# Performance work log

Measured on AMD Instinct MI355X. Metric: run time of the kernel, lower is better.

Reference implementation:

```python
import jax, jax.numpy as jnp
import numpy as np

B, S, HID, NH, DH = 2, 1024, 4096, 32, 128
ACT_BITS, W_BITS = 8, 4
NEG_INF = float(np.finfo(np.float32).min)


def _qdq(x, bits):
    """Symmetric fake-quant over the last axis (per-token / per-out-channel), with STE."""
    qmax = 2.0 ** (bits - 1) - 1
    s = jnp.maximum(jnp.max(jnp.abs(x), axis=-1, keepdims=True) / qmax, 1e-8)
    q = jnp.clip(jnp.round(x / s), -qmax - 1, qmax) * s
    return x + jax.lax.stop_gradient(q - x)


def _rope_tables(seq_len, dim):
    inv_freq = 1.0 / (10000.0 ** (np.arange(0, dim, 2, dtype=np.float32) / dim))
    t = np.arange(seq_len, dtype=np.float32)
    freqs = np.outer(t, inv_freq)              # [S, DH/2]
    emb = np.concatenate([freqs, freqs], -1)   # [S, DH]
    return jnp.asarray(np.cos(emb)), jnp.asarray(np.sin(emb))


def _rotate_half(x):
    h = x.shape[-1] // 2
    return jnp.concatenate([-x[..., h:], x[..., :h]], axis=-1)


def _norm(x):
    return jnp.linalg.norm(x, axis=-1, keepdims=True)


def setup_inputs() -> dict:
    key = jax.random.key(0)
    ks = jax.random.split(key, 5)
    causal = jnp.where(jnp.tril(jnp.ones((S, S), dtype=bool)), 0.0, NEG_INF).astype(jnp.float32)
    return {
        "hidden_states": jax.random.normal(ks[0], (B, S, HID), jnp.float32),
        "wq": jax.random.normal(ks[1], (HID, HID), jnp.float32) * 0.02,
        "wk": jax.random.normal(ks[2], (HID, HID), jnp.float32) * 0.02,
        "wv": jax.random.normal(ks[3], (HID, HID), jnp.float32) * 0.02,
        "wo": jax.random.normal(ks[4], (HID, HID), jnp.float32) * 0.02,
        "attention_mask": jnp.broadcast_to(causal[None, None], (B, 1, S, S)),
    }


def reference(hidden_states, wq, wk, wv, wo, attention_mask):
    cos, sin = _rope_tables(S, DH)
    cos, sin = cos[None, None], sin[None, None]          # [1,1,S,DH]
    x = _qdq(hidden_states, ACT_BITS)                    # act fake-quant (per token)

    def proj(w):
        return jnp.einsum('bsh,dh->bsd', x, _qdq(w, W_BITS)).reshape(B, S, NH, DH).transpose(0, 2, 1, 3)

    q, k, v = proj(wq), proj(wk), proj(wv)               # [B,H,S,D]
    q = q * cos + _rotate_half(q) * sin
    k = k * cos + _rotate_half(k) * sin

    # qkt_matmul: quant Q and K, rescale scores by quantization norm ratios a1, a2
    x1len = _norm(q)
    qq = _qdq(q, ACT_BITS)
    a1 = _norm(qq) / x1len                               # [B,H,S,1]
    x2len = _norm(k)
    kq = _qdq(k, ACT_BITS)
    a2 = jnp.swapaxes(_norm(kq) / x2len, 2, 3)           # [B,H,1,S]

    attn = jnp.einsum('bhqd,bhkd->bhqk', qq, kq) / np.float32(np.sqrt(DH))
    attn = attn / a1 / a2
    attn = attn + attention_mask
    attn = jnp.maximum(attn, NEG_INF)
    p = jax.nn.softmax(attn.astype(jnp.float32), axis=-1)

    # pv_matmul: quant P and V, rescale output by V's norm ratio
    pq = _qdq(p, ACT_BITS)
    x2len_v = _norm(v)
    vq = _qdq(v, ACT_BITS)
    a2v = _norm(vq) / x2len_v                            # [B,H,S,1]

    out = jnp.einsum('bhqk,bhkd->bhqd', pq, vq) / a2v    # [B,H,S,D]
    out = out.transpose(0, 2, 1, 3).reshape(B, S, HID)
    out = jnp.einsum('bsh,dh->bsd', _qdq(out, ACT_BITS), _qdq(wo, W_BITS))
    return out
```

## Files before the change

### kernel.cpp

```cpp
#include <hip/hip_runtime.h>
#include <hip/hip_bf16.h>
#include <math.h>
#include <stdint.h>

#define NEG_INF_F (-3.4028234663852886e38f)

typedef __bf16 bf16_t;
typedef __bf16 bf16x8 __attribute__((ext_vector_type(8)));
typedef float f32x4 __attribute__((ext_vector_type(4)));
typedef float f32x16 __attribute__((ext_vector_type(16)));
typedef int i32x4 __attribute__((ext_vector_type(4)));
typedef int i32x16 __attribute__((ext_vector_type(16)));
typedef int8_t c8x4 __attribute__((ext_vector_type(4)));

static constexpr int Bb = 2, Ss = 1024, Hid = 4096, Nh = 32, Dh = 128;
static constexpr int Mr = Bb * Ss;
static constexpr int Bh = Bb * Nh;

__device__ __forceinline__ void gload_lds16(const void* g, void* l) {
  __builtin_amdgcn_global_load_lds((const __attribute__((address_space(1))) void*)g,
                                   (__attribute__((address_space(3))) void*)l, 16, 0, 0);
}

__device__ __forceinline__ float wred_max(float v) {
#pragma unroll
  for (int off = 32; off > 0; off >>= 1) v = fmaxf(v, __shfl_xor(v, off));
  return v;
}

__device__ __forceinline__ unsigned pkbf(float a, float b) {
  unsigned short ua = __builtin_bit_cast(unsigned short, (bf16_t)a);
  unsigned short ub = __builtin_bit_cast(unsigned short, (bf16_t)b);
  return (unsigned)ua | ((unsigned)ub << 16);
}

__global__ void rope_table_kernel(float* __restrict__ ctab, float* __restrict__ stab) {
  int i = blockIdx.x * 256 + threadIdx.x;
  int srow = i >> 6, d = i & 63;
  float invf = (float)pow(10000.0, -((double)(2 * d) / (double)Dh));
  float ang = (float)srow * invf;
  ctab[i] = (float)cos((double)ang);
  stab[i] = (float)sin((double)ang);
}

__device__ __forceinline__ void quant_row_body(
    const float* __restrict__ x, int8_t* __restrict__ o, float* __restrict__ scale,
    int row, int ncols, float qmax, float clo, float chi)
{
  const int tid = threadIdx.x;
  const float4* x4 = (const float4*)x;
  const int n4 = ncols >> 2;
  float m = 0.f;
  for (int i = tid; i < n4; i += 256) {
    float4 v = x4[i];
    m = fmaxf(m, fmaxf(fmaxf(fabsf(v.x), fabsf(v.y)), fmaxf(fabsf(v.z), fabsf(v.w))));
  }
  m = wred_max(m);
  __shared__ float red[4];
  if ((tid & 63) == 0) red[tid >> 6] = m;
  __syncthreads();
  m = fmaxf(fmaxf(red[0], red[1]), fmaxf(red[2], red[3]));
  const float s = fmaxf(m / qmax, 1e-8f);
  if (tid == 0) scale[row] = s;
  c8x4* o4 = (c8x4*)o;
  for (int i = tid; i < n4; i += 256) {
    float4 v = x4[i];
    c8x4 r;
    r[0] = (int8_t)(int)fminf(fmaxf(rintf(v.x / s), clo), chi);
    r[1] = (int8_t)(int)fminf(fmaxf(rintf(v.y / s), clo), chi);
    r[2] = (int8_t)(int)fminf(fmaxf(rintf(v.z / s), clo), chi);
    r[3] = (int8_t)(int)fminf(fmaxf(rintf(v.w / s), clo), chi);
    o4[i] = r;
  }
}

__global__ __launch_bounds__(256) void quant_rows_kernel(
    const float* __restrict__ in, int8_t* __restrict__ outq,
    float* __restrict__ scale, int ncols, float qmax, float clo, float chi)
{
  const int row = blockIdx.x;
  quant_row_body(in + (size_t)row * ncols, outq + (size_t)row * ncols, scale,
                 row, ncols, qmax, clo, chi);
}

__global__ __launch_bounds__(256) void quant_w3_kernel(
    const float* __restrict__ w0, const float* __restrict__ w1, const float* __restrict__ w2,
    int8_t* __restrict__ o0, int8_t* __restrict__ o1, int8_t* __restrict__ o2,
    float* __restrict__ s0, float* __restrict__ s1, float* __restrict__ s2)
{
  const int sel = blockIdx.x >> 12, row = blockIdx.x & 4095;
  const float* in = sel == 0 ? w0 : (sel == 1 ? w1 : w2);
  int8_t* o = sel == 0 ? o0 : (sel == 1 ? o1 : o2);
  float* sc = sel == 0 ? s0 : (sel == 1 ? s1 : s2);
  quant_row_body(in + (size_t)row * Hid, o + (size_t)row * Hid, sc, row, Hid,
                 7.f, -8.f, 7.f);
}

__global__ __launch_bounds__(256) void qkv_gemm_kernel(
    const int8_t* __restrict__ A, const float* __restrict__ sA,
    const int8_t* __restrict__ wqz, const int8_t* __restrict__ wkz, const int8_t* __restrict__ wvz,
    const float* __restrict__ swq, const float* __restrict__ swk, const float* __restrict__ swv,
    int8_t* __restrict__ qqb, float* __restrict__ Fq,
    int8_t* __restrict__ kqb, float* __restrict__ Fk,
    bf16_t* __restrict__ vdq, float* __restrict__ a2vp,
    const float* __restrict__ ctab, const float* __restrict__ stab)
{
  __shared__ __align__(16) char smem[34816 + 3072];
  int8_t* As = (int8_t*)smem;
  int8_t* Bs = (int8_t*)(smem + 16384);
  float (*s_red)[128][3] = (float (*)[128][3])(smem + 34816);

  const int tid = threadIdx.x, lane = tid & 63, wid = tid >> 6;
  const int id = blockIdx.x;
  const int xcd = id & 7, within = id >> 3;
  const int nIdx = xcd * 12 + (within >> 4);
  const int mIdx = within & 15;
  const int wsel = nIdx >> 5, head = nIdx & 31;
  const int bm = mIdx * 128, bn = head * 128;
  const int8_t* W = wsel == 0 ? wqz : (wsel == 1 ? wkz : wvz);
  const float* sW = wsel == 0 ? swq : (wsel == 1 ? swk : swv);
  constexpr int K = Hid;

  const int wm = wid >> 1, wn = wid & 1;
  const int l15 = lane & 15, kg4 = lane >> 4;

  const int strow = wid * 8 + (lane >> 3);
  const int schunk = ((lane & 7) ^ (lane >> 3)) * 16;
  const int8_t* gA = A + (size_t)(bm + strow) * K + schunk;
  const int8_t* gB = W + (size_t)(bn + strow) * K + schunk;

  i32x4 acc[4][4] = {};
  for (int k0 = 0; k0 < K; k0 += 128) {
    if (k0) __syncthreads();
#pragma unroll
    for (int r = 0; r < 4; ++r) {
      gload_lds16(gA + k0 + (size_t)r * 32 * K, As + r * 4096 + wid * 1024);
      gload_lds16(gB + k0 + (size_t)r * 32 * K, Bs + r * 4096 + wid * 1024);
    }
    __syncthreads();
#pragma unroll
    for (int g = 0; g < 2; ++g) {
      i32x4 af[4], bw[4];
#pragma unroll
      for (int f = 0; f < 4; ++f) {
        const int ca = (((g << 2) | kg4) ^ (l15 & 7)) * 16;
        af[f] = *(const i32x4*)&As[(wm * 64 + f * 16 + l15) * 128 + ca];
        bw[f] = *(const i32x4*)&Bs[(f * 32 + wn * 16 + l15) * 128 + ca];
      }
#pragma unroll
      for (int fm = 0; fm < 4; ++fm)
#pragma unroll
        for (int fn = 0; fn < 4; ++fn)
          acc[fm][fn] = __builtin_amdgcn_mfma_i32_16x16x64_i8(af[fm], bw[fn], acc[fm][fn], 0, 0, 0);
    }
  }

  float sav[4][4], swv_[4];
#pragma unroll
  for (int fm = 0; fm < 4; ++fm)
#pragma unroll
    for (int j = 0; j < 4; ++j) sav[fm][j] = sA[bm + wm * 64 + fm * 16 + kg4 * 4 + j];
#pragma unroll
  for (int fn = 0; fn < 4; ++fn) swv_[fn] = sW[bn + fn * 32 + wn * 16 + l15];

  float val[4][4][4];
#pragma unroll
  for (int fm = 0; fm < 4; ++fm)
#pragma unroll
    for (int fn = 0; fn < 4; ++fn)
#pragma unroll
      for (int j = 0; j < 4; ++j)
        val[fm][fn][j] = (float)acc[fm][fn][j] * sav[fm][j] * swv_[fn];

  const int b = bm >> 10;
  const int bh = b * Nh + head;
  float r_[4][4][4];
  if (wsel != 2) {
    const int dmA = wn * 16 + l15, dmB = 32 + wn * 16 + l15;
#pragma unroll
    for (int fm = 0; fm < 4; ++fm)
#pragma unroll
      for (int j = 0; j < 4; ++j) {
        const int srow = (bm + wm * 64 + fm * 16 + kg4 * 4 + j) & (Ss - 1);
        const float cA = ctab[srow * 64 + dmA], cB = ctab[srow * 64 + dmB];
        const float sA_ = stab[srow * 64 + dmA], sB_ = stab[srow * 64 + dmB];
        r_[fm][0][j] = __fsub_rn(__fmul_rn(val[fm][0][j], cA), __fmul_rn(val[fm][2][j], sA_));
        r_[fm][1][j] = __fsub_rn(__fmul_rn(val[fm][1][j], cB), __fmul_rn(val[fm][3][j], sB_));
        r_[fm][2][j] = __fadd_rn(__fmul_rn(val[fm][2][j], cA), __fmul_rn(val[fm][0][j], sA_));
        r_[fm][3][j] = __fadd_rn(__fmul_rn(val[fm][3][j], cB), __fmul_rn(val[fm][1][j], sB_));
      }
  } else {
#pragma unroll
    for (int fm = 0; fm < 4; ++fm)
#pragma unroll
      for (int fn = 0; fn < 4; ++fn)
#pragma unroll
        for (int j = 0; j < 4; ++j) r_[fm][fn][j] = val[fm][fn][j];
  }
  float ma_[4][4], n2_[4][4];
#pragma unroll
  for (int fm = 0; fm < 4; ++fm)
#pragma unroll
    for (int j = 0; j < 4; ++j) {
      float ma = 0.f, n2 = 0.f;
#pragma unroll
      for (int fn = 0; fn < 4; ++fn) {
        const float x = r_[fm][fn][j];
        ma = fmaxf(ma, fabsf(x));
        n2 += x * x;
      }
#pragma unroll
      for (int off = 1; off < 16; off <<= 1) {
        ma = fmaxf(ma, __shfl_xor(ma, off));
        n2 += __shfl_xor(n2, off);
      }
      ma_[fm][j] = ma;
      n2_[fm][j] = n2;
    }
  if (l15 == 0) {
#pragma unroll
    for (int fm = 0; fm < 4; ++fm)
#pragma unroll
      for (int j = 0; j < 4; ++j) {
        const int rl = wm * 64 + fm * 16 + kg4 * 4 + j;
        s_red[wn][rl][0] = ma_[fm][j];
        s_red[wn][rl][1] = n2_[fm][j];
      }
  }
  __syncthreads();
  float qc[4][4][4], svl[4][4], n2c[4][4], nq2_[4][4];
#pragma unroll
  for (int fm = 0; fm < 4; ++fm)
#pragma unroll
    for (int j = 0; j < 4; ++j) {
      const int rl = wm * 64 + fm * 16 + kg4 * 4 + j;
      const float ma = fmaxf(ma_[fm][j], s_red[wn ^ 1][rl][0]);
      const float n2 = n2_[fm][j] + s_red[wn ^ 1][rl][1];
      const float s = fmaxf(ma / 127.0f, 1e-8f);
      float nq2 = 0.f;
#pragma unroll
      for (int fn = 0; fn < 4; ++fn) {
        const float q = fminf(fmaxf(rintf(r_[fm][fn][j] / s), -128.f), 127.f);
        qc[fm][fn][j] = q;
        nq2 += q * q;
      }
#pragma unroll
      for (int off = 1; off < 16; off <<= 1) nq2 += __shfl_xor(nq2, off);
      svl[fm][j] = s;
      n2c[fm][j] = n2;
      nq2_[fm][j] = nq2;
    }
  __syncthreads();
  if (l15 == 0) {
#pragma unroll
    for (int fm = 0; fm < 4; ++fm)
#pragma unroll
      for (int j = 0; j < 4; ++j)
        s_red[wn][wm * 64 + fm * 16 + kg4 * 4 + j][2] = nq2_[fm][j];
  }
  __syncthreads();

  if (wsel != 2) {
    int8_t* outq = (wsel == 0) ? qqb : kqb;
    float* Ff = (wsel == 0) ? Fq : Fk;
#pragma unroll
    for (int fm = 0; fm < 4; ++fm)
#pragma unroll
      for (int j = 0; j < 4; ++j) {
        const int rl = wm * 64 + fm * 16 + kg4 * 4 + j;
        const int stok = (bm + rl) & (Ss - 1);
        const size_t rowBase = ((size_t)bh * Ss + stok) * Dh;
#pragma unroll
        for (int fn = 0; fn < 4; ++fn)
          outq[rowBase + fn * 32 + wn * 16 + l15] = (int8_t)(int)qc[fm][fn][j];
        if (wn == 0 && l15 == 0) {
          const float nq2 = nq2_[fm][j] + s_red[1][rl][2];
          Ff[(size_t)bh * Ss + stok] = sqrtf(n2c[fm][j] / nq2) * 0.2973017787506803f;
        }
      }
  } else {
    bf16_t* svt = (bf16_t*)smem;
#pragma unroll
    for (int fm = 0; fm < 4; ++fm)
#pragma unroll
      for (int j = 0; j < 4; ++j) {
        const int t = wm * 64 + fm * 16 + kg4 * 4 + j;
#pragma unroll
        for (int fn = 0; fn < 4; ++fn) {
          const int d = fn * 32 + wn * 16 + l15;
          svt[d * 136 + t] = (bf16_t)(qc[fm][fn][j] * svl[fm][j]);
        }
        if (wn == 0 && l15 == 0) {
          const float nq2 = nq2_[fm][j] + s_red[1][t][2];
          a2vp[(size_t)bh * Ss + ((bm + t) & (Ss - 1))] =
              svl[fm][j] * sqrtf(nq2) / sqrtf(n2c[fm][j]);
        }
      }
    __syncthreads();
    const int d = tid >> 1, toff = (tid & 1) * 64;
    const int s0 = bm & (Ss - 1);
    const bf16_t* src = svt + d * 136 + toff;
    bf16_t* dst = vdq + ((size_t)bh * Dh + d) * Ss + s0 + toff;
#pragma unroll
    for (int k = 0; k < 8; ++k) {
      bf16x8 tv;
#pragma unroll
      for (int e = 0; e < 8; ++e) tv[e] = src[k * 8 + e];
      *(bf16x8*)(dst + k * 8) = tv;
    }
  }
}

__global__ __launch_bounds__(256) void gemm0_kernel(
    const int8_t* __restrict__ A, const float* __restrict__ sA,
    const int8_t* __restrict__ W, const float* __restrict__ sW,
    float* __restrict__ out, int M, int N, int K)
{
  __shared__ __align__(16) int8_t As[128 * 128];
  __shared__ __align__(16) int8_t Bs[128 * 128];
  const int tid = threadIdx.x, lane = tid & 63, wid = tid >> 6;
  const int id = blockIdx.x;
  const int xcd = id & 7, within = id >> 3;
  const int nIdx = xcd * 4 + (within >> 4);
  const int mIdx = within & 15;
  const int bm = mIdx * 128, bn = nIdx * 128;
  const int wm = wid >> 1, wn = wid & 1;
  const int l15 = lane & 15, kg4 = lane >> 4;

  const int strow = wid * 8 + (lane >> 3);
  const int schunk = ((lane & 7) ^ (lane >> 3)) * 16;
  const int8_t* gA = A + (size_t)(bm + strow) * K + schunk;
  const int8_t* gB = W + (size_t)(bn + strow) * K + schunk;

  i32x4 acc[4][4] = {};
  for (int k0 = 0; k0 < K; k0 += 128) {
    if (k0) __syncthreads();
#pragma unroll
    for (int r = 0; r < 4; ++r) {
      gload_lds16(gA + k0 + (size_t)r * 32 * K, As + r * 4096 + wid * 1024);
      gload_lds16(gB + k0 + (size_t)r * 32 * K, Bs + r * 4096 + wid * 1024);
    }
    __syncthreads();
#pragma unroll
    for (int g = 0; g < 2; ++g) {
      i32x4 af[4], bw[4];
#pragma unroll
      for (int f = 0; f < 4; ++f) {
        const int ca = (((g << 2) | kg4) ^ (l15 & 7)) * 16;
        af[f] = *(const i32x4*)&As[(wm * 64 + f * 16 + l15) * 128 + ca];
        bw[f] = *(const i32x4*)&Bs[(f * 32 + wn * 16 + l15) * 128 + ca];
      }
#pragma unroll
      for (int fm = 0; fm < 4; ++fm)
#pragma unroll
        for (int fn = 0; fn < 4; ++fn)
          acc[fm][fn] = __builtin_amdgcn_mfma_i32_16x16x64_i8(af[fm], bw[fn], acc[fm][fn], 0, 0, 0);
    }
  }
#pragma unroll
  for (int fm = 0; fm < 4; ++fm) {
#pragma unroll
    for (int j = 0; j < 4; ++j) {
      const int row = bm + wm * 64 + fm * 16 + kg4 * 4 + j;
      const float sa = sA[row];
#pragma unroll
      for (int fn = 0; fn < 4; ++fn) {
        const int col = bn + fn * 32 + wn * 16 + l15;
        out[(size_t)row * N + col] = (float)acc[fm][fn][j] * sa * sW[col];
      }
    }
  }
}

#define KR(r) (((r) & 3) + 8 * ((r) >> 2) + 4 * hi)
__global__ __launch_bounds__(64, 2) void attn_kernel(
    const int8_t* __restrict__ qq, const int8_t* __restrict__ kq,
    const bf16_t* __restrict__ vdqt,
    const float* __restrict__ Fq, const float* __restrict__ Fk,
    const float* __restrict__ A2v, float* __restrict__ oattn)
{
  const int bh = blockIdx.x, b = bh >> 5, h = bh & 31;
  const int lane = threadIdx.x & 63;
  const int l31 = lane & 31, hi = lane >> 5;
  const int u = 31 - (int)blockIdx.y;
  const int q0 = u * 32;
  const int nt = u + 1;
  const size_t bhS = (size_t)bh * Ss;

  const int8_t* qrow = qq + (bhS + q0 + l31) * Dh + hi * 16;
  i32x4 qf[4];
#pragma unroll
  for (int c = 0; c < 4; ++c) qf[c] = *(const i32x4*)(qrow + c * 32);
  const float fq = Fq[bhS + q0 + l31];
  const int qcol = q0 + l31;

  float m = NEG_INF_F;
  int t = 0;
  for (; t + 1 < nt; t += 2) {
    const int kb0 = t * 32, kb1 = kb0 + 32;
    const int8_t* kr0 = kq + (bhS + kb0 + l31) * Dh + hi * 16;
    const int8_t* kr1 = kq + (bhS + kb1 + l31) * Dh + hi * 16;
    i32x16 ca = {}, cb = {}, da = {}, db = {};
    ca = __builtin_amdgcn_mfma_i32_32x32x32_i8(*(const i32x4*)(kr0),      qf[0], ca, 0, 0, 0);
    cb = __builtin_amdgcn_mfma_i32_32x32x32_i8(*(const i32x4*)(kr0 + 64), qf[2], cb, 0, 0, 0);
    da = __builtin_amdgcn_mfma_i32_32x32x32_i8(*(const i32x4*)(kr1),      qf[0], da, 0, 0, 0);
    db = __builtin_amdgcn_mfma_i32_32x32x32_i8(*(const i32x4*)(kr1 + 64), qf[2], db, 0, 0, 0);
    ca = __builtin_amdgcn_mfma_i32_32x32x32_i8(*(const i32x4*)(kr0 + 32), qf[1], ca, 0, 0, 0);
    cb = __builtin_amdgcn_mfma_i32_32x32x32_i8(*(const i32x4*)(kr0 + 96), qf[3], cb, 0, 0, 0);
    da = __builtin_amdgcn_mfma_i32_32x32x32_i8(*(const i32x4*)(kr1 + 32), qf[1], da, 0, 0, 0);
    db = __builtin_amdgcn_mfma_i32_32x32x32_i8(*(const i32x4*)(kr1 + 96), qf[3], db, 0, 0, 0);
    float4 fk40[4], fk41[4];
#pragma unroll
    for (int g = 0; g < 4; ++g) fk40[g] = *(const float4*)&Fk[bhS + kb0 + g * 8 + 4 * hi];
#pragma unroll
    for (int g = 0; g < 4; ++g) fk41[g] = *(const float4*)&Fk[bhS + kb1 + g * 8 + 4 * hi];
    const bool diag1 = (t + 1 == nt - 1);
#pragma unroll
    for (int r = 0; r < 16; ++r) {
      m = fmaxf(m, (float)(ca[r] + cb[r]) * fq * ((const float*)&fk40[r >> 2])[r & 3]);
      const float v1 = (float)(da[r] + db[r]) * fq * ((const float*)&fk41[r >> 2])[r & 3];
      if (!diag1 || (kb1 + KR(r) <= qcol)) m = fmaxf(m, v1);
    }
  }
  if (t < nt) {
    const int kb = t * 32;
    const int8_t* krow = kq + (bhS + kb + l31) * Dh + hi * 16;
    i32x16 ca = {}, cb = {};
    ca = __builtin_amdgcn_mfma_i32_32x32x32_i8(*(const i32x4*)(krow),      qf[0], ca, 0, 0, 0);
    cb = __builtin_amdgcn_mfma_i32_32x32x32_i8(*(const i32x4*)(krow + 64), qf[2], cb, 0, 0, 0);
    ca = __builtin_amdgcn_mfma_i32_32x32x32_i8(*(const i32x4*)(krow + 32), qf[1], ca, 0, 0, 0);
    cb = __builtin_amdgcn_mfma_i32_32x32x32_i8(*(const i32x4*)(krow + 96), qf[3], cb, 0, 0, 0);
    float4 fk4[4];
#pragma unroll
    for (int g = 0; g < 4; ++g) fk4[g] = *(const float4*)&Fk[bhS + kb + g * 8 + 4 * hi];
#pragma unroll
    for (int r = 0; r < 16; ++r) {
      const float v = (float)(ca[r] + cb[r]) * fq * ((const float*)&fk4[r >> 2])[r & 3];
      if (kb + KR(r) <= qcol) m = fmaxf(m, v);
    }
  }
  m = fmaxf(m, __shfl_xor(m, 32));

  float z = 0.f;
  f32x16 oacc[4] = {};
  for (int tt = 0; tt < nt; ++tt) {
    const int kb = tt * 32;
    const int8_t* krow = kq + (bhS + kb + l31) * Dh + hi * 16;
    i32x16 ca = {}, cb = {};
    ca = __builtin_amdgcn_mfma_i32_32x32x32_i8(*(const i32x4*)(krow),      qf[0], ca, 0, 0, 0);
    cb = __builtin_amdgcn_mfma_i32_32x32x32_i8(*(const i32x4*)(krow + 64), qf[2], cb, 0, 0, 0);
    ca = __builtin_amdgcn_mfma_i32_32x32x32_i8(*(const i32x4*)(krow + 32), qf[1], ca, 0, 0, 0);
    cb = __builtin_amdgcn_mfma_i32_32x32x32_i8(*(const i32x4*)(krow + 96), qf[3], cb, 0, 0, 0);
    float4 fk4[4];
#pragma unroll
    for (int g = 0; g < 4; ++g) fk4[g] = *(const float4*)&Fk[bhS + kb + g * 8 + 4 * hi];
    float p[16];
    const bool diag = (tt == nt - 1);
#pragma unroll
    for (int r = 0; r < 16; ++r) {
      float v = (float)(ca[r] + cb[r]) * fq * ((const float*)&fk4[r >> 2])[r & 3];
      if (diag && (kb + KR(r) > qcol)) v = NEG_INF_F;
      const float e = __expf(v - m);
      z += e;
      p[r] = rintf(127.0f * e);
    }
#pragma unroll
    for (int s = 0; s < 2; ++s) {
      const int rs = s * 8;
      unsigned k0 = pkbf(p[rs + 0], p[rs + 1]);
      unsigned k1 = pkbf(p[rs + 2], p[rs + 3]);
      unsigned k2 = pkbf(p[rs + 4], p[rs + 5]);
      unsigned k3 = pkbf(p[rs + 6], p[rs + 7]);
      unsigned sx0 = __shfl_xor(k0, 32);
      unsigned sx1 = __shfl_xor(k1, 32);
      unsigned sx2 = __shfl_xor(k2, 32);
      unsigned sx3 = __shfl_xor(k3, 32);
      uint4 ww;
      ww.x = hi ? sx2 : k0;
      ww.y = hi ? sx3 : k1;
      ww.z = hi ? k2 : sx0;
      ww.w = hi ? k3 : sx1;
      const bf16x8 af = __builtin_bit_cast(bf16x8, ww);
      const int kg2 = kb + s * 16 + hi * 8;
#pragma unroll
      for (int dt = 0; dt < 4; ++dt) {
        const bf16x8 vf = *(const bf16x8*)(vdqt + ((size_t)bh * Dh + dt * 32 + l31) * Ss + kg2);
        oacc[dt] = __builtin_amdgcn_mfma_f32_32x32x16_bf16(af, vf, oacc[dt], 0, 0, 0);
      }
    }
  }
  z += __shfl_xor(z, 32);
  const float osc = (1.0f / z) / 127.0f / A2v[bhS + q0 + l31];
#pragma unroll
  for (int dt = 0; dt < 4; ++dt) {
#pragma unroll
    for (int r = 0; r < 16; ++r) {
      const int q = q0 + KR(r);
      const float oscr = __shfl(osc, KR(r));
      oattn[((size_t)b * Ss + q) * Hid + h * Dh + dt * 32 + l31] = oacc[dt][r] * oscr;
    }
  }
}

extern "C" void kernel_launch(void* const* d_in, const int* in_sizes, int n_in,
                              void* d_out, int out_size, void* d_ws, size_t ws_size,
                              hipStream_t stream)
{
  const float* hidden = (const float*)d_in[0];
  const float* wq = (const float*)d_in[1];
  const float* wk = (const float*)d_in[2];
  const float* wv = (const float*)d_in[3];
  const float* wo = (const float*)d_in[4];
  float* out = (float*)d_out;

  char* p = (char*)d_ws;
  auto alloc = [&](size_t bytes) -> char* {
    char* r = p; p += (bytes + 255) & ~(size_t)255; return r;
  };
  int8_t* xq   = (int8_t*)alloc((size_t)Mr * Hid);
  int8_t* wb0  = (int8_t*)alloc((size_t)Hid * Hid);
  int8_t* wb1  = (int8_t*)alloc((size_t)Hid * Hid);
  int8_t* wb2  = (int8_t*)alloc((size_t)Hid * Hid);
  float*  oat  = (float*) alloc((size_t)Bh * Ss * Dh * sizeof(float));
  int8_t* qqb  = (int8_t*)alloc((size_t)Bh * Ss * Dh);
  int8_t* kqb  = (int8_t*)alloc((size_t)Bh * Ss * Dh);
  bf16_t* vdqt = (bf16_t*)alloc((size_t)Bh * Dh * Ss * sizeof(bf16_t));
  float* sxa = (float*)alloc((size_t)Mr * sizeof(float));
  float* sw0 = (float*)alloc((size_t)Hid * sizeof(float));
  float* sw1 = (float*)alloc((size_t)Hid * sizeof(float));
  float* sw2 = (float*)alloc((size_t)Hid * sizeof(float));
  float* Fq  = (float*)alloc((size_t)Bh * Ss * sizeof(float));
  float* Fk  = (float*)alloc((size_t)Bh * Ss * sizeof(float));
  float* A2v = (float*)alloc((size_t)Bh * Ss * sizeof(float));
  float* soa = (float*)alloc((size_t)Mr * sizeof(float));
  float* ctab = (float*)alloc((size_t)Ss * 64 * sizeof(float));
  float* stab = (float*)alloc((size_t)Ss * 64 * sizeof(float));
  int8_t* oq  = xq;

  rope_table_kernel<<<Ss * 64 / 256, 256, 0, stream>>>(ctab, stab);
  quant_rows_kernel<<<Mr, 256, 0, stream>>>(hidden, xq, sxa, Hid, 127.f, -128.f, 127.f);
  quant_w3_kernel<<<3 * Hid, 256, 0, stream>>>(wq, wk, wv, wb0, wb1, wb2, sw0, sw1, sw2);

  qkv_gemm_kernel<<<1536, 256, 0, stream>>>(xq, sxa, wb0, wb1, wb2, sw0, sw1, sw2,
                                            qqb, Fq, kqb, Fk, vdqt, A2v, ctab, stab);

  dim3 ga(Bh, 32);
  attn_kernel<<<ga, 64, 0, stream>>>(qqb, kqb, vdqt, Fq, Fk, A2v, oat);

  quant_rows_kernel<<<Mr, 256, 0, stream>>>(oat, oq, soa, Hid, 127.f, -128.f, 127.f);
  quant_rows_kernel<<<Hid, 256, 0, stream>>>(wo, wb0, sw0, Hid, 7.f, -8.f, 7.f);
  gemm0_kernel<<<512, 256, 0, stream>>>(oq, soa, wb0, sw0, out, Mr, Hid, Hid);
}
```

Before: 366.2 us.

## Double-buffer int8 GEMM main loops and split attention key tiles across four waves

Result: slower. 392.6 us (+7.2%).

```diff
diff --git a/kernel.cpp b/kernel.cpp
--- a/kernel.cpp
+++ b/kernel.cpp
@@ -96,6 +96,50 @@
                  7.f, -8.f, 7.f);
 }
 
+#define GEMM_CORE_DBUF(SMEM)                                                          \
+  int8_t* A0 = (int8_t*)(SMEM);                                                       \
+  int8_t* A1 = (int8_t*)(SMEM) + 8192;                                                \
+  int8_t* B0 = (int8_t*)(SMEM) + 16384;                                               \
+  int8_t* B1 = (int8_t*)(SMEM) + 24576;                                               \
+  const int srowL = tid >> 2;                                                         \
+  const int schunk = ((tid & 3) ^ ((tid >> 3) & 3)) * 16;                             \
+  const int8_t* gA = A + (size_t)(bm + srowL) * K + schunk;                           \
+  const int8_t* gB = W + (size_t)(bn + srowL) * K + schunk;                           \
+  const size_t rstep = (size_t)64 * K;                                                \
+  const int ck = (kg4 ^ ((l15 >> 1) & 3)) * 16;                                       \
+  i32x4 acc[4][4] = {};                                                               \
+  {                                                                                   \
+    gload_lds16(gA, A0 + wid * 1024);                                                 \
+    gload_lds16(gA + rstep, A0 + 4096 + wid * 1024);                                  \
+    gload_lds16(gB, B0 + wid * 1024);                                                 \
+    gload_lds16(gB + rstep, B0 + 4096 + wid * 1024);                                  \
+    __syncthreads();                                                                  \
+    int8_t *Ac = A0, *An = A1, *Bc = B0, *Bn = B1;                                    \
+    for (int k0 = 0; k0 < K; k0 += 64) {                                              \
+      if (k0 + 64 < K) {                                                              \
+        gload_lds16(gA + k0 + 64, An + wid * 1024);                                   \
+        gload_lds16(gA + k0 + 64 + rstep, An + 4096 + wid * 1024);                    \
+        gload_lds16(gB + k0 + 64, Bn + wid * 1024);                                   \
+        gload_lds16(gB + k0 + 64 + rstep, Bn + 4096 + wid * 1024);                    \
+      }                                                                               \
+      i32x4 af[4], bw[4];                                                             \
+      _Pragma("unroll")                                                               \
+      for (int f = 0; f < 4; ++f) {                                                   \
+        af[f] = *(const i32x4*)&Ac[(wm * 64 + f * 16 + l15) * 64 + ck];               \
+        bw[f] = *(const i32x4*)&Bc[(f * 32 + wn * 16 + l15) * 64 + ck];               \
+      }                                                                               \
+      _Pragma("unroll")                                                               \
+      for (int fm = 0; fm < 4; ++fm)                                                  \
+        _Pragma("unroll")                                                             \
+        for (int fn = 0; fn < 4; ++fn)                                                \
+          acc[fm][fn] = __builtin_amdgcn_mfma_i32_16x16x64_i8(af[fm], bw[fn],         \
+                                                              acc[fm][fn], 0, 0, 0); \
+      __syncthreads();                                                                \
+      int8_t* t_ = Ac; Ac = An; An = t_;                                              \
+      t_ = Bc; Bc = Bn; Bn = t_;                                                      \
+    }                                                                                 \
+  }
+
 __global__ __launch_bounds__(256) void qkv_gemm_kernel(
     const int8_t* __restrict__ A, const float* __restrict__ sA,
     const int8_t* __restrict__ wqz, const int8_t* __restrict__ wkz, const int8_t* __restrict__ wvz,
@@ -106,8 +150,6 @@
     const float* __restrict__ ctab, const float* __restrict__ stab)
 {
   __shared__ __align__(16) char smem[34816 + 3072];
-  int8_t* As = (int8_t*)smem;
-  int8_t* Bs = (int8_t*)(smem + 16384);
   float (*s_red)[128][3] = (float (*)[128][3])(smem + 34816);
 
   const int tid = threadIdx.x, lane = tid & 63, wid = tid >> 6;
@@ -124,36 +166,7 @@
   const int wm = wid >> 1, wn = wid & 1;
   const int l15 = lane & 15, kg4 = lane >> 4;
 
-  const int strow = wid * 8 + (lane >> 3);
-  const int schunk = ((lane & 7) ^ (lane >> 3)) * 16;
-  const int8_t* gA = A + (size_t)(bm + strow) * K + schunk;
-  const int8_t* gB = W + (size_t)(bn + strow) * K + schunk;
-
-  i32x4 acc[4][4] = {};
-  for (int k0 = 0; k0 < K; k0 += 128) {
-    if (k0) __syncthreads();
-#pragma unroll
-    for (int r = 0; r < 4; ++r) {
-      gload_lds16(gA + k0 + (size_t)r * 32 * K, As + r * 4096 + wid * 1024);
-      gload_lds16(gB + k0 + (size_t)r * 32 * K, Bs + r * 4096 + wid * 1024);
-    }
-    __syncthreads();
-#pragma unroll
-    for (int g = 0; g < 2; ++g) {
-      i32x4 af[4], bw[4];
-#pragma unroll
-      for (int f = 0; f < 4; ++f) {
-        const int ca = (((g << 2) | kg4) ^ (l15 & 7)) * 16;
-        af[f] = *(const i32x4*)&As[(wm * 64 + f * 16 + l15) * 128 + ca];
-        bw[f] = *(const i32x4*)&Bs[(f * 32 + wn * 16 + l15) * 128 + ca];
-      }
-#pragma unroll
-      for (int fm = 0; fm < 4; ++fm)
-#pragma unroll
-        for (int fn = 0; fn < 4; ++fn)
-          acc[fm][fn] = __builtin_amdgcn_mfma_i32_16x16x64_i8(af[fm], bw[fn], acc[fm][fn], 0, 0, 0);
-    }
-  }
+  GEMM_CORE_DBUF(smem)
 
   float sav[4][4], swv_[4];
 #pragma unroll
@@ -316,8 +329,7 @@
     const int8_t* __restrict__ W, const float* __restrict__ sW,
     float* __restrict__ out, int M, int N, int K)
 {
-  __shared__ __align__(16) int8_t As[128 * 128];
-  __shared__ __align__(16) int8_t Bs[128 * 128];
+  __shared__ __align__(16) char smem[32768];
   const int tid = threadIdx.x, lane = tid & 63, wid = tid >> 6;
   const int id = blockIdx.x;
   const int xcd = id & 7, within = id >> 3;
@@ -327,36 +339,8 @@
   const int wm = wid >> 1, wn = wid & 1;
   const int l15 = lane & 15, kg4 = lane >> 4;
 
-  const int strow = wid * 8 + (lane >> 3);
-  const int schunk = ((lane & 7) ^ (lane >> 3)) * 16;
-  const int8_t* gA = A + (size_t)(bm + strow) * K + schunk;
-  const int8_t* gB = W + (size_t)(bn + strow) * K + schunk;
-
-  i32x4 acc[4][4] = {};
-  for (int k0 = 0; k0 < K; k0 += 128) {
-    if (k0) __syncthreads();
-#pragma unroll
-    for (int r = 0; r < 4; ++r) {
-      gload_lds16(gA + k0 + (size_t)r * 32 * K, As + r * 4096 + wid * 1024);
-      gload_lds16(gB + k0 + (size_t)r * 32 * K, Bs + r * 4096 + wid * 1024);
-    }
-    __syncthreads();
-#pragma unroll
-    for (int g = 0; g < 2; ++g) {
-      i32x4 af[4], bw[4];
-#pragma unroll
-      for (int f = 0; f < 4; ++f) {
-        const int ca = (((g << 2) | kg4) ^ (l15 & 7)) * 16;
-        af[f] = *(const i32x4*)&As[(wm * 64 + f * 16 + l15) * 128 + ca];
-        bw[f] = *(const i32x4*)&Bs[(f * 32 + wn * 16 + l15) * 128 + ca];
-      }
-#pragma unroll
-      for (int fm = 0; fm < 4; ++fm)
-#pragma unroll
-        for (int fn = 0; fn < 4; ++fn)
-          acc[fm][fn] = __builtin_amdgcn_mfma_i32_16x16x64_i8(af[fm], bw[fn], acc[fm][fn], 0, 0, 0);
-    }
-  }
+  GEMM_CORE_DBUF(smem)
+
 #pragma unroll
   for (int fm = 0; fm < 4; ++fm) {
 #pragma unroll
@@ -373,20 +357,24 @@
 }
 
 #define KR(r) (((r) & 3) + 8 * ((r) >> 2) + 4 * hi)
-__global__ __launch_bounds__(64, 2) void attn_kernel(
+__global__ __launch_bounds__(256, 2) void attn_kernel(
     const int8_t* __restrict__ qq, const int8_t* __restrict__ kq,
     const bf16_t* __restrict__ vdqt,
     const float* __restrict__ Fq, const float* __restrict__ Fk,
     const float* __restrict__ A2v, float* __restrict__ oattn)
 {
   const int bh = blockIdx.x, b = bh >> 5, h = bh & 31;
-  const int lane = threadIdx.x & 63;
+  const int tid = threadIdx.x, lane = tid & 63, wid = tid >> 6;
   const int l31 = lane & 31, hi = lane >> 5;
   const int u = 31 - (int)blockIdx.y;
   const int q0 = u * 32;
   const int nt = u + 1;
   const size_t bhS = (size_t)bh * Ss;
 
+  __shared__ float s_m[4][32];
+  __shared__ float s_z[4][32];
+  __shared__ float s_acc[2][64][65];
+
   const int8_t* qrow = qq + (bhS + q0 + l31) * Dh + hi * 16;
   i32x4 qf[4];
 #pragma unroll
@@ -395,34 +383,7 @@
   const int qcol = q0 + l31;
 
   float m = NEG_INF_F;
-  int t = 0;
-  for (; t + 1 < nt; t += 2) {
-    const int kb0 = t * 32, kb1 = kb0 + 32;
-    const int8_t* kr0 = kq + (bhS + kb0 + l31) * Dh + hi * 16;
-    const int8_t* kr1 = kq + (bhS + kb1 + l31) * Dh + hi * 16;
-    i32x16 ca = {}, cb = {}, da = {}, db = {};
-    ca = __builtin_amdgcn_mfma_i32_32x32x32_i8(*(const i32x4*)(kr0),      qf[0], ca, 0, 0, 0);
-    cb = __builtin_amdgcn_mfma_i32_32x32x32_i8(*(const i32x4*)(kr0 + 64), qf[2], cb, 0, 0, 0);
-    da = __builtin_amdgcn_mfma_i32_32x32x32_i8(*(const i32x4*)(kr1),      qf[0], da, 0, 0, 0);
-    db = __builtin_amdgcn_mfma_i32_32x32x32_i8(*(const i32x4*)(kr1 + 64), qf[2], db, 0, 0, 0);
-    ca = __builtin_amdgcn_mfma_i32_32x32x32_i8(*(const i32x4*)(kr0 + 32), qf[1], ca, 0, 0, 0);
-    cb = __builtin_amdgcn_mfma_i32_32x32x32_i8(*(const i32x4*)(kr0 + 96), qf[3], cb, 0, 0, 0);
-    da = __builtin_amdgcn_mfma_i32_32x32x32_i8(*(const i32x4*)(kr1 + 32), qf[1], da, 0, 0, 0);
-    db = __builtin_amdgcn_mfma_i32_32x32x32_i8(*(const i32x4*)(kr1 + 96), qf[3], db, 0, 0, 0);
-    float4 fk40[4], fk41[4];
-#pragma unroll
-    for (int g = 0; g < 4; ++g) fk40[g] = *(const float4*)&Fk[bhS + kb0 + g * 8 + 4 * hi];
-#pragma unroll
-    for (int g = 0; g < 4; ++g) fk41[g] = *(const float4*)&Fk[bhS + kb1 + g * 8 + 4 * hi];
-    const bool diag1 = (t + 1 == nt - 1);
-#pragma unroll
-    for (int r = 0; r < 16; ++r) {
-      m = fmaxf(m, (float)(ca[r] + cb[r]) * fq * ((const float*)&fk40[r >> 2])[r & 3]);
-      const float v1 = (float)(da[r] + db[r]) * fq * ((const float*)&fk41[r >> 2])[r & 3];
-      if (!diag1 || (kb1 + KR(r) <= qcol)) m = fmaxf(m, v1);
-    }
-  }
-  if (t < nt) {
+  for (int t = wid; t < nt; t += 4) {
     const int kb = t * 32;
     const int8_t* krow = kq + (bhS + kb + l31) * Dh + hi * 16;
     i32x16 ca = {}, cb = {};
@@ -433,18 +394,22 @@
     float4 fk4[4];
 #pragma unroll
     for (int g = 0; g < 4; ++g) fk4[g] = *(const float4*)&Fk[bhS + kb + g * 8 + 4 * hi];
+    const bool diag = (t == nt - 1);
 #pragma unroll
     for (int r = 0; r < 16; ++r) {
       const float v = (float)(ca[r] + cb[r]) * fq * ((const float*)&fk4[r >> 2])[r & 3];
-      if (kb + KR(r) <= qcol) m = fmaxf(m, v);
+      if (!diag || (kb + KR(r) <= qcol)) m = fmaxf(m, v);
     }
   }
   m = fmaxf(m, __shfl_xor(m, 32));
+  if (lane < 32) s_m[wid][l31] = m;
+  __syncthreads();
+  m = fmaxf(fmaxf(s_m[0][l31], s_m[1][l31]), fmaxf(s_m[2][l31], s_m[3][l31]));
 
   float z = 0.f;
   f32x16 oacc[4] = {};
-  for (int tt = 0; tt < nt; ++tt) {
-    const int kb = tt * 32;
+  for (int t = wid; t < nt; t += 4) {
+    const int kb = t * 32;
     const int8_t* krow = kq + (bhS + kb + l31) * Dh + hi * 16;
     i32x16 ca = {}, cb = {};
     ca = __builtin_amdgcn_mfma_i32_32x32x32_i8(*(const i32x4*)(krow),      qf[0], ca, 0, 0, 0);
@@ -455,7 +420,7 @@
 #pragma unroll
     for (int g = 0; g < 4; ++g) fk4[g] = *(const float4*)&Fk[bhS + kb + g * 8 + 4 * hi];
     float p[16];
-    const bool diag = (tt == nt - 1);
+    const bool diag = (t == nt - 1);
 #pragma unroll
     for (int r = 0; r < 16; ++r) {
       float v = (float)(ca[r] + cb[r]) * fq * ((const float*)&fk4[r >> 2])[r & 3];
@@ -490,14 +455,35 @@
     }
   }
   z += __shfl_xor(z, 32);
-  const float osc = (1.0f / z) / 127.0f / A2v[bhS + q0 + l31];
-#pragma unroll
-  for (int dt = 0; dt < 4; ++dt) {
-#pragma unroll
-    for (int r = 0; r < 16; ++r) {
-      const int q = q0 + KR(r);
-      const float oscr = __shfl(osc, KR(r));
-      oattn[((size_t)b * Ss + q) * Hid + h * Dh + dt * 32 + l31] = oacc[dt][r] * oscr;
+  if (lane < 32) s_z[wid][l31] = z;
+  if (wid >= 2) {
+#pragma unroll
+    for (int e = 0; e < 64; ++e) s_acc[wid - 2][e][lane] = oacc[e >> 4][e & 15];
+  }
+  __syncthreads();
+  if (wid < 2) {
+#pragma unroll
+    for (int e = 0; e < 64; ++e) oacc[e >> 4][e & 15] += s_acc[wid][e][lane];
+  }
+  __syncthreads();
+  if (wid == 1) {
+#pragma unroll
+    for (int e = 0; e < 64; ++e) s_acc[0][e][lane] = oacc[e >> 4][e & 15];
+  }
+  __syncthreads();
+  if (wid == 0) {
+#pragma unroll
+    for (int e = 0; e < 64; ++e) oacc[e >> 4][e & 15] += s_acc[0][e][lane];
+    const float zt = (s_z[0][l31] + s_z[1][l31]) + (s_z[2][l31] + s_z[3][l31]);
+    const float osc = (1.0f / zt) / 127.0f / A2v[bhS + q0 + l31];
+#pragma unroll
+    for (int dt = 0; dt < 4; ++dt) {
+#pragma unroll
+      for (int r = 0; r < 16; ++r) {
+        const int q = q0 + KR(r);
+        const float oscr = __shfl(osc, KR(r));
+        oattn[((size_t)b * Ss + q) * Hid + h * Dh + dt * 32 + l31] = oacc[dt][r] * oscr;
+      }
     }
   }
 }
@@ -545,7 +531,7 @@
                                             qqb, Fq, kqb, Fk, vdqt, A2v, ctab, stab);
 
   dim3 ga(Bh, 32);
-  attn_kernel<<<ga, 64, 0, stream>>>(qqb, kqb, vdqt, Fq, Fk, A2v, oat);
+  attn_kernel<<<ga, 256, 0, stream>>>(qqb, kqb, vdqt, Fq, Fk, A2v, oat);
 
   quant_rows_kernel<<<Mr, 256, 0, stream>>>(oat, oq, soa, Hid, 127.f, -128.f, 127.f);
   quant_rows_kernel<<<Hid, 256, 0, stream>>>(wo, wb0, sw0, Hid, 7.f, -8.f, 7.f);
```

## Double-buffer int8 GEMM LDS tiles with 64-wide K stages to overlap loads

Applied to the files above, without the earlier changes.

New measurement: 391.4 us. 6.9% more time.

```diff
diff --git a/kernel.cpp b/kernel.cpp
--- a/kernel.cpp
+++ b/kernel.cpp
@@ -96,6 +96,51 @@
                  7.f, -8.f, 7.f);
 }
 
+#define GEMM_PHASE(Abuf, Bbuf)                                                        \
+  {                                                                                   \
+    i32x4 af[4], bw[4];                                                               \
+    _Pragma("unroll")                                                                 \
+    for (int f = 0; f < 4; ++f) {                                                     \
+      af[f] = *(const i32x4*)&(Abuf)[(wm * 64 + f * 16 + l15) * 64 + ck];             \
+      bw[f] = *(const i32x4*)&(Bbuf)[(f * 32 + wn * 16 + l15) * 64 + ck];             \
+    }                                                                                 \
+    _Pragma("unroll")                                                                 \
+    for (int fm = 0; fm < 4; ++fm)                                                    \
+      _Pragma("unroll")                                                               \
+      for (int fn = 0; fn < 4; ++fn)                                                  \
+        acc[fm][fn] = __builtin_amdgcn_mfma_i32_16x16x64_i8(af[fm], bw[fn],           \
+                                                            acc[fm][fn], 0, 0, 0);   \
+  }
+
+#define GEMM_STAGE(koff, Abuf, Bbuf)                                                  \
+  gload_lds16(gA + (koff), (Abuf) + wid * 1024);                                      \
+  gload_lds16(gA + (koff) + rstep, (Abuf) + 4096 + wid * 1024);                       \
+  gload_lds16(gB + (koff), (Bbuf) + wid * 1024);                                      \
+  gload_lds16(gB + (koff) + rstep, (Bbuf) + 4096 + wid * 1024);
+
+#define GEMM_CORE_DBUF(SMEM)                                                          \
+  int8_t* A0 = (int8_t*)(SMEM);                                                       \
+  int8_t* A1 = (int8_t*)(SMEM) + 8192;                                                \
+  int8_t* B0 = (int8_t*)(SMEM) + 16384;                                               \
+  int8_t* B1 = (int8_t*)(SMEM) + 24576;                                               \
+  const int srowL = tid >> 2;                                                         \
+  const int schunk = ((tid & 3) ^ ((tid >> 3) & 3)) * 16;                             \
+  const int8_t* gA = A + (size_t)(bm + srowL) * K + schunk;                           \
+  const int8_t* gB = W + (size_t)(bn + srowL) * K + schunk;                           \
+  const size_t rstep = (size_t)64 * K;                                                \
+  const int ck = (kg4 ^ ((l15 >> 1) & 3)) * 16;                                       \
+  i32x4 acc[4][4] = {};                                                               \
+  GEMM_STAGE(0, A0, B0)                                                               \
+  __syncthreads();                                                                    \
+  for (int k0 = 0; k0 < K; k0 += 128) {                                               \
+    if (k0 + 64 < K) { GEMM_STAGE(k0 + 64, A1, B1) }                                  \
+    GEMM_PHASE(A0, B0)                                                                \
+    __syncthreads();                                                                  \
+    if (k0 + 128 < K) { GEMM_STAGE(k0 + 128, A0, B0) }                                \
+    GEMM_PHASE(A1, B1)                                                                \
+    __syncthreads();                                                                  \
+  }
+
 __global__ __launch_bounds__(256) void qkv_gemm_kernel(
     const int8_t* __restrict__ A, const float* __restrict__ sA,
     const int8_t* __restrict__ wqz, const int8_t* __restrict__ wkz, const int8_t* __restrict__ wvz,
@@ -106,8 +151,6 @@
     const float* __restrict__ ctab, const float* __restrict__ stab)
 {
   __shared__ __align__(16) char smem[34816 + 3072];
-  int8_t* As = (int8_t*)smem;
-  int8_t* Bs = (int8_t*)(smem + 16384);
   float (*s_red)[128][3] = (float (*)[128][3])(smem + 34816);
 
   const int tid = threadIdx.x, lane = tid & 63, wid = tid >> 6;
@@ -124,36 +167,7 @@
   const int wm = wid >> 1, wn = wid & 1;
   const int l15 = lane & 15, kg4 = lane >> 4;
 
-  const int strow = wid * 8 + (lane >> 3);
-  const int schunk = ((lane & 7) ^ (lane >> 3)) * 16;
-  const int8_t* gA = A + (size_t)(bm + strow) * K + schunk;
-  const int8_t* gB = W + (size_t)(bn + strow) * K + schunk;
-
-  i32x4 acc[4][4] = {};
-  for (int k0 = 0; k0 < K; k0 += 128) {
-    if (k0) __syncthreads();
-#pragma unroll
-    for (int r = 0; r < 4; ++r) {
-      gload_lds16(gA + k0 + (size_t)r * 32 * K, As + r * 4096 + wid * 1024);
-      gload_lds16(gB + k0 + (size_t)r * 32 * K, Bs + r * 4096 + wid * 1024);
-    }
-    __syncthreads();
-#pragma unroll
-    for (int g = 0; g < 2; ++g) {
-      i32x4 af[4], bw[4];
-#pragma unroll
-      for (int f = 0; f < 4; ++f) {
-        const int ca = (((g << 2) | kg4) ^ (l15 & 7)) * 16;
-        af[f] = *(const i32x4*)&As[(wm * 64 + f * 16 + l15) * 128 + ca];
-        bw[f] = *(const i32x4*)&Bs[(f * 32 + wn * 16 + l15) * 128 + ca];
-      }
-#pragma unroll
-      for (int fm = 0; fm < 4; ++fm)
-#pragma unroll
-        for (int fn = 0; fn < 4; ++fn)
-          acc[fm][fn] = __builtin_amdgcn_mfma_i32_16x16x64_i8(af[fm], bw[fn], acc[fm][fn], 0, 0, 0);
-    }
-  }
+  GEMM_CORE_DBUF(smem)
 
   float sav[4][4], swv_[4];
 #pragma unroll
@@ -316,8 +330,7 @@
     const int8_t* __restrict__ W, const float* __restrict__ sW,
     float* __restrict__ out, int M, int N, int K)
 {
-  __shared__ __align__(16) int8_t As[128 * 128];
-  __shared__ __align__(16) int8_t Bs[128 * 128];
+  __shared__ __align__(16) char smem[32768];
   const int tid = threadIdx.x, lane = tid & 63, wid = tid >> 6;
   const int id = blockIdx.x;
   const int xcd = id & 7, within = id >> 3;
@@ -327,36 +340,8 @@
   const int wm = wid >> 1, wn = wid & 1;
   const int l15 = lane & 15, kg4 = lane >> 4;
 
-  const int strow = wid * 8 + (lane >> 3);
-  const int schunk = ((lane & 7) ^ (lane >> 3)) * 16;
-  const int8_t* gA = A + (size_t)(bm + strow) * K + schunk;
-  const int8_t* gB = W + (size_t)(bn + strow) * K + schunk;
-
-  i32x4 acc[4][4] = {};
-  for (int k0 = 0; k0 < K; k0 += 128) {
-    if (k0) __syncthreads();
-#pragma unroll
-    for (int r = 0; r < 4; ++r) {
-      gload_lds16(gA + k0 + (size_t)r * 32 * K, As + r * 4096 + wid * 1024);
-      gload_lds16(gB + k0 + (size_t)r * 32 * K, Bs + r * 4096 + wid * 1024);
-    }
-    __syncthreads();
-#pragma unroll
-    for (int g = 0; g < 2; ++g) {
-      i32x4 af[4], bw[4];
-#pragma unroll
-      for (int f = 0; f < 4; ++f) {
-        const int ca = (((g << 2) | kg4) ^ (l15 & 7)) * 16;
-        af[f] = *(const i32x4*)&As[(wm * 64 + f * 16 + l15) * 128 + ca];
-        bw[f] = *(const i32x4*)&Bs[(f * 32 + wn * 16 + l15) * 128 + ca];
-      }
-#pragma unroll
-      for (int fm = 0; fm < 4; ++fm)
-#pragma unroll
-        for (int fn = 0; fn < 4; ++fn)
-          acc[fm][fn] = __builtin_amdgcn_mfma_i32_16x16x64_i8(af[fm], bw[fn], acc[fm][fn], 0, 0, 0);
-    }
-  }
+  GEMM_CORE_DBUF(smem)
+
 #pragma unroll
   for (int fm = 0; fm < 4; ++fm) {
 #pragma unroll
```
